# Performance work log

Hardware: AMD Instinct MI355X
Metric: run time of the kernel (lower is better)

Reference implementation:

```python
import jax, jax.numpy as jnp
import numpy as np

B, N, K, F_IN, F_OUT = 8, 2048, 32, 256, 256


def setup_inputs() -> dict:
    key = jax.random.key(0)
    ks = jax.random.split(key, 8)
    x = jax.random.normal(ks[0], (B, N, F_IN), dtype=jnp.float32)
    idx_neib = jax.random.randint(ks[1], (N, K), 0, N, dtype=jnp.int32)
    # Linear params (torch nn.Linear stores weight as [out, in])
    lim_x = np.sqrt(2.0) * np.sqrt(6.0 / (F_IN + F_OUT))  # xavier_uniform, gain=relu
    Wx_w = jax.random.uniform(ks[2], (F_OUT, F_IN), jnp.float32, -lim_x, lim_x)
    Wx_b = jnp.zeros((F_OUT,), jnp.float32)
    Wn_w = jax.random.uniform(ks[3], (F_OUT, F_IN), jnp.float32, -lim_x, lim_x)
    Wn_b = jnp.zeros((F_OUT,), jnp.float32)
    gamma = jnp.ones((2 * F_OUT,), jnp.float32)
    beta = jnp.zeros((2 * F_OUT,), jnp.float32)
    return {"x": x, "idx_neib": idx_neib, "Wx_w": Wx_w, "Wx_b": Wx_b,
            "Wn_w": Wn_w, "Wn_b": Wn_b, "gamma": gamma, "beta": beta}


def reference(x, idx_neib, Wx_w, Wx_b, Wn_w, Wn_b, gamma, beta):
    # Gather neighbor features: [B, N, K, F] then mean over the K neighbors.
    x_neib = jnp.take(x, idx_neib, axis=1).mean(axis=2)  # [B, N, F]
    # Dual linear projections (weights stored [out, in] as in torch).
    h_self = jnp.einsum('bnf,of->bno', x, Wx_w) + Wx_b
    h_nei = jnp.einsum('bnf,of->bno', x_neib, Wn_w) + Wn_b
    h = jnp.concatenate([h_self, h_nei], axis=2)          # [B, N, 2*out]
    # F.normalize(p=2, dim=2): divide by max(||h||_2, 1e-12)
    nrm = jnp.sqrt(jnp.sum(h * h, axis=2, keepdims=True))
    h = h / jnp.maximum(nrm, 1e-12)
    h = jax.nn.relu(h)
    # BatchNorm1d over channel dim (training mode: batch stats over B and N,
    # biased variance), eps=1e-5.
    mu = h.mean(axis=(0, 1))
    var = jnp.mean((h - mu) ** 2, axis=(0, 1))
    h = (h - mu) * jax.lax.rsqrt(var + 1e-5) * gamma + beta
    return h
```

## Files before the change

kernel.cpp:

```cpp
#include <hip/hip_runtime.h>
#include <stdint.h>

#define BB 8
#define NN 2048
#define KK 32
#define FIN 256
#define FOUT 256
#define CC 512
#define MM (BB*NN)
#define RB 32
#define NBLK (MM/RB)
#define LDA 264

typedef __attribute__((ext_vector_type(8))) short short8;
typedef __attribute__((ext_vector_type(4))) float f32x4;

__device__ __forceinline__ unsigned short f2bf(float f) {
    union { float f; unsigned u; } v; v.f = f;
    unsigned u = v.u;
    return (unsigned short)((u + 0x7FFFu + ((u >> 16) & 1u)) >> 16);
}
__device__ __forceinline__ float bf2f(unsigned short s) {
    union { unsigned u; float f; } v; v.u = ((unsigned)s) << 16;
    return v.f;
}

__global__ void k_prep(const float* __restrict__ Wx, const float* __restrict__ Wxb,
                       const float* __restrict__ Wn, const float* __restrict__ Wnb,
                       const float* __restrict__ x,
                       unsigned short* __restrict__ Wc, float* __restrict__ bc,
                       unsigned short* __restrict__ xb) {
    const int blk = blockIdx.x;
    const int tid = threadIdx.x;
    if (blk < 128) {
        int gid = blk * 256 + tid;
        int e0 = gid * 4;
        int o = e0 >> 8, k = e0 & 255;
        const float* src = (o < FOUT) ? (Wx + o * FIN + k) : (Wn + (o - FOUT) * FIN + k);
        float4 v = *(const float4*)src;
        ushort4 p; p.x = f2bf(v.x); p.y = f2bf(v.y); p.z = f2bf(v.z); p.w = f2bf(v.w);
        *(ushort4*)(Wc + e0) = p;
        if (gid < 128) {
            int c0 = gid * 4;
            float4 bv = (c0 < FOUT) ? *(const float4*)(Wxb + c0)
                                    : *(const float4*)(Wnb + c0 - FOUT);
            *(float4*)(bc + c0) = bv;
        }
    } else {
        size_t gid = (size_t)(blk - 128) * 256 + tid;
        size_t e0 = gid * 8;
        float4 v0 = *(const float4*)(x + e0);
        float4 v1 = *(const float4*)(x + e0 + 4);
        ushort4 p0, p1;
        p0.x = f2bf(v0.x); p0.y = f2bf(v0.y); p0.z = f2bf(v0.z); p0.w = f2bf(v0.w);
        p1.x = f2bf(v1.x); p1.y = f2bf(v1.y); p1.z = f2bf(v1.z); p1.w = f2bf(v1.w);
        *(ushort4*)(xb + e0)     = p0;
        *(ushort4*)(xb + e0 + 4) = p1;
    }
}

__global__ __launch_bounds__(512, 4)
void k_gemm(const unsigned short* __restrict__ xb, const int* __restrict__ idx,
            const unsigned short* __restrict__ Wc,
            const float* __restrict__ bc,
            unsigned short* __restrict__ h,
            float* __restrict__ psum, float* __restrict__ psq) {
    __shared__ unsigned short As[2][RB * LDA];
    __shared__ float sqpart[8][RB];
    __shared__ float rnorm[RB];

    const int bid  = blockIdx.x;
    const int tid  = threadIdx.x;
    const int w    = tid >> 6;
    const int lane = tid & 63;
    const int quad = lane >> 4;
    const int l16  = lane & 15;
    const int p    = lane >> 5;
    const int l32  = lane & 31;
    const int b    = bid & 7;
    const int n0   = (bid >> 3) * RB;
    const unsigned short* xbat = xb + (size_t)b * NN * FIN;
    const size_t r0g = (size_t)b * NN + n0;

    {
        const uint4* gs = (const uint4*)(xbat + (size_t)n0 * FIN);
        #pragma unroll
        for (int i = 0; i < 2; ++i) {
            int e = tid + i * 512;
            *(uint4*)&As[0][(e >> 5) * LDA + (e & 31) * 8] = gs[e];
        }
    }
    {
        #pragma unroll
        for (int rr = 0; rr < 4; ++rr) {
            int lr = (w << 2) + rr;
            const int* ip = idx + (n0 + lr) * KK;
            const unsigned short* xp = xbat + l32 * 8;
            float ac[8] = {0.f,0.f,0.f,0.f,0.f,0.f,0.f,0.f};
            #pragma unroll 8
            for (int k = 0; k < 16; ++k) {
                int j = ip[(k << 1) | p];
                uint4 v = *(const uint4*)(xp + (size_t)j * FIN);
                const unsigned short* hv = (const unsigned short*)&v;
                #pragma unroll
                for (int c = 0; c < 8; ++c) ac[c] += bf2f(hv[c]);
            }
            #pragma unroll
            for (int c = 0; c < 8; ++c) ac[c] += __shfl_xor(ac[c], 32, 64);
            if (p == 0) {
                const float s = 1.0f / (float)KK;
                unsigned short o8[8];
                #pragma unroll
                for (int c = 0; c < 8; ++c) o8[c] = f2bf(ac[c] * s);
                *(uint4*)&As[1][lr * LDA + l32 * 8] = *(const uint4*)o8;
            }
        }
    }
    __syncthreads();

    const int half = w >> 2;
    const unsigned short* A = As[half];
    const int cbg = half * 256 + (w & 3) * 64;

    f32x4 acc[2][4];
    #pragma unroll
    for (int mt = 0; mt < 2; ++mt)
        #pragma unroll
        for (int nt = 0; nt < 4; ++nt) acc[mt][nt] = (f32x4){0.f, 0.f, 0.f, 0.f};

    const unsigned short* Bp = Wc + (size_t)(cbg + l16) * FIN + quad * 8;
    const unsigned short* Ap = A + (size_t)l16 * LDA + quad * 8;

    #pragma unroll 2
    for (int k0 = 0; k0 < FIN; k0 += 32) {
        short8 a0 = *(const short8*)(Ap + k0);
        short8 a1 = *(const short8*)(Ap + 16 * LDA + k0);
        short8 bfr[4];
        #pragma unroll
        for (int nt = 0; nt < 4; ++nt)
            bfr[nt] = *(const short8*)(Bp + (size_t)nt * 16 * FIN + k0);
        #pragma unroll
        for (int nt = 0; nt < 4; ++nt) {
            acc[0][nt] = __builtin_amdgcn_mfma_f32_16x16x32_bf16(a0, bfr[nt], acc[0][nt], 0, 0, 0);
            acc[1][nt] = __builtin_amdgcn_mfma_f32_16x16x32_bf16(a1, bfr[nt], acc[1][nt], 0, 0, 0);
        }
    }

    float bcv[4];
    #pragma unroll
    for (int nt = 0; nt < 4; ++nt) bcv[nt] = bc[cbg + nt * 16 + l16];

    float rsq[2][4] = {{0.f,0.f,0.f,0.f},{0.f,0.f,0.f,0.f}};
    #pragma unroll
    for (int mt = 0; mt < 2; ++mt)
        #pragma unroll
        for (int nt = 0; nt < 4; ++nt)
            #pragma unroll
            for (int r = 0; r < 4; ++r) {
                float v = acc[mt][nt][r] + bcv[nt];
                acc[mt][nt][r] = v;
                rsq[mt][r] += v * v;
            }
    #pragma unroll
    for (int off = 1; off < 16; off <<= 1)
        #pragma unroll
        for (int mt = 0; mt < 2; ++mt)
            #pragma unroll
            for (int r = 0; r < 4; ++r)
                rsq[mt][r] += __shfl_xor(rsq[mt][r], off, 64);
    if (l16 == 0) {
        #pragma unroll
        for (int mt = 0; mt < 2; ++mt)
            #pragma unroll
            for (int r = 0; r < 4; ++r)
                sqpart[w][mt * 16 + quad * 4 + r] = rsq[mt][r];
    }
    __syncthreads();
    if (tid < RB) {
        float tot = 0.f;
        #pragma unroll
        for (int i = 0; i < 8; ++i) tot += sqpart[i][tid];
        rnorm[tid] = 1.0f / fmaxf(sqrtf(tot), 1e-12f);
    }
    __syncthreads();

    float csum[4] = {0.f,0.f,0.f,0.f};
    float csq [4] = {0.f,0.f,0.f,0.f};
    #pragma unroll
    for (int mt = 0; mt < 2; ++mt) {
        #pragma unroll
        for (int r = 0; r < 4; ++r) {
            int row = mt * 16 + quad * 4 + r;
            float rn = rnorm[row];
            unsigned short* hp = h + (r0g + row) * CC + cbg + l16;
            #pragma unroll
            for (int nt = 0; nt < 4; ++nt) {
                float v = fmaxf(acc[mt][nt][r] * rn, 0.0f);
                hp[nt * 16] = f2bf(v);
                csum[nt] += v;
                csq [nt] += v * v;
            }
        }
    }
    #pragma unroll
    for (int off = 16; off < 64; off <<= 1)
        #pragma unroll
        for (int nt = 0; nt < 4; ++nt) {
            csum[nt] += __shfl_xor(csum[nt], off, 64);
            csq [nt] += __shfl_xor(csq [nt], off, 64);
        }
    if (quad == 0) {
        #pragma unroll
        for (int nt = 0; nt < 4; ++nt) {
            int c = cbg + nt * 16 + l16;
            psum[(size_t)c * NBLK + bid] = csum[nt];
            psq [(size_t)c * NBLK + bid] = csq [nt];
        }
    }
}

__global__ void k_stats(const float* __restrict__ psum, const float* __restrict__ psq,
                        const float* __restrict__ gamma, const float* __restrict__ beta,
                        float* __restrict__ ss) {
    __shared__ float ps[4], pq[4];
    int c = blockIdx.x, t = threadIdx.x;
    float s = psum[(size_t)c * NBLK + t] + psum[(size_t)c * NBLK + 256 + t];
    float q = psq [(size_t)c * NBLK + t] + psq [(size_t)c * NBLK + 256 + t];
    #pragma unroll
    for (int off = 32; off; off >>= 1) { s += __shfl_xor(s, off, 64); q += __shfl_xor(q, off, 64); }
    int w = t >> 6, lane = t & 63;
    if (lane == 0) { ps[w] = s; pq[w] = q; }
    __syncthreads();
    if (t == 0) {
        float S = ps[0] + ps[1] + ps[2] + ps[3];
        float Q = pq[0] + pq[1] + pq[2] + pq[3];
        const float inv = 1.0f / (float)MM;
        float mu  = S * inv;
        float var = fmaxf(Q * inv - mu * mu, 0.0f);
        float sc  = gamma[c] * rsqrtf(var + 1e-5f);
        ss[c]      = sc;
        ss[CC + c] = beta[c] - mu * sc;
    }
}

__global__ void k_apply(const unsigned short* __restrict__ h,
                        const float* __restrict__ ss,
                        float* __restrict__ out) {
    int gid = blockIdx.x * 256 + threadIdx.x;
    int c0 = (gid * 8) & (CC - 1);
    uint4 hv = ((const uint4*)h)[gid];
    const unsigned short* hs = (const unsigned short*)&hv;
    float4 sc0 = *(const float4*)(ss + c0);
    float4 sc1 = *(const float4*)(ss + c0 + 4);
    float4 sh0 = *(const float4*)(ss + CC + c0);
    float4 sh1 = *(const float4*)(ss + CC + c0 + 4);
    float4 o0, o1;
    o0.x = bf2f(hs[0]) * sc0.x + sh0.x;
    o0.y = bf2f(hs[1]) * sc0.y + sh0.y;
    o0.z = bf2f(hs[2]) * sc0.z + sh0.z;
    o0.w = bf2f(hs[3]) * sc0.w + sh0.w;
    o1.x = bf2f(hs[4]) * sc1.x + sh1.x;
    o1.y = bf2f(hs[5]) * sc1.y + sh1.y;
    o1.z = bf2f(hs[6]) * sc1.z + sh1.z;
    o1.w = bf2f(hs[7]) * sc1.w + sh1.w;
    ((float4*)out)[gid * 2]     = o0;
    ((float4*)out)[gid * 2 + 1] = o1;
}

extern "C" void kernel_launch(void* const* d_in, const int* in_sizes, int n_in,
                              void* d_out, int out_size, void* d_ws, size_t ws_size,
                              hipStream_t stream) {
    const float* x     = (const float*)d_in[0];
    const int*   idx   = (const int*)  d_in[1];
    const float* Wx_w  = (const float*)d_in[2];
    const float* Wx_b  = (const float*)d_in[3];
    const float* Wn_w  = (const float*)d_in[4];
    const float* Wn_b  = (const float*)d_in[5];
    const float* gamma = (const float*)d_in[6];
    const float* beta  = (const float*)d_in[7];
    float* out = (float*)d_out;

    char* p = (char*)d_ws;
    unsigned short* xb = (unsigned short*)p; p += (size_t)MM * FIN * 2;
    unsigned short* Wc = (unsigned short*)p; p += (size_t)CC * FIN * 2;
    float* bc          = (float*)p;          p += (size_t)CC * 4;
    unsigned short* h  = (unsigned short*)p; p += (size_t)MM * CC * 2;
    float* psum        = (float*)p;          p += (size_t)CC * NBLK * 4;
    float* psq         = (float*)p;          p += (size_t)CC * NBLK * 4;
    float* ss          = (float*)p;          p += (size_t)2 * CC * 4;

    hipLaunchKernelGGL(k_prep,  dim3(2176), dim3(256), 0, stream,
                       Wx_w, Wx_b, Wn_w, Wn_b, x, Wc, bc, xb);
    hipLaunchKernelGGL(k_gemm,  dim3(NBLK), dim3(512), 0, stream, xb, idx, Wc, bc, h, psum, psq);
    hipLaunchKernelGGL(k_stats, dim3(CC),   dim3(256), 0, stream, psum, psq, gamma, beta, ss);
    hipLaunchKernelGGL(k_apply, dim3(4096), dim3(256), 0, stream, h, ss, out);
}
```

Baseline: 130.4 us.

## Transpose bf16 activations to node-major layout so neighbor gathers cover all batches

The prep kernel now writes the bf16 copy of x as [N][B][F] instead of [B][N][F]. Each GEMM block takes 4 nodes across all 8 batches (32 rows), so one neighbor index fetches a contiguous 4 KB slab covering every batch. This cuts index loads and turns scattered 512-byte row gathers into larger coalesced reads. Output row addressing and the per-block stat partials are remapped to match. The cost is a strided scatter in the prep kernel's store pattern.

```diff
diff --git a/kernel.cpp b/kernel.cpp
--- a/kernel.cpp
+++ b/kernel.cpp
@@ -9,7 +9,7 @@
 #define CC 512
 #define MM (BB*NN)
 #define RB 32
-#define NBLK (MM/RB)
+#define NBLK 512
 #define LDA 264
 
 typedef __attribute__((ext_vector_type(8))) short short8;
@@ -29,7 +29,7 @@
                        const float* __restrict__ Wn, const float* __restrict__ Wnb,
                        const float* __restrict__ x,
                        unsigned short* __restrict__ Wc, float* __restrict__ bc,
-                       unsigned short* __restrict__ xb) {
+                       unsigned short* __restrict__ xb_t) {
     const int blk = blockIdx.x;
     const int tid = threadIdx.x;
     if (blk < 128) {
@@ -49,18 +49,22 @@
     } else {
         size_t gid = (size_t)(blk - 128) * 256 + tid;
         size_t e0 = gid * 8;
+        int b = (int)(e0 >> 19);
+        int n = (int)((e0 >> 8) & (NN - 1));
+        int c = (int)(e0 & (FIN - 1));
         float4 v0 = *(const float4*)(x + e0);
         float4 v1 = *(const float4*)(x + e0 + 4);
         ushort4 p0, p1;
         p0.x = f2bf(v0.x); p0.y = f2bf(v0.y); p0.z = f2bf(v0.z); p0.w = f2bf(v0.w);
         p1.x = f2bf(v1.x); p1.y = f2bf(v1.y); p1.z = f2bf(v1.z); p1.w = f2bf(v1.w);
-        *(ushort4*)(xb + e0)     = p0;
-        *(ushort4*)(xb + e0 + 4) = p1;
+        unsigned short* dst = xb_t + ((size_t)n * BB + b) * FIN + c;
+        *(ushort4*)dst       = p0;
+        *(ushort4*)(dst + 4) = p1;
     }
 }
 
 __global__ __launch_bounds__(512, 4)
-void k_gemm(const unsigned short* __restrict__ xb, const int* __restrict__ idx,
+void k_gemm(const unsigned short* __restrict__ xb_t, const int* __restrict__ idx,
             const unsigned short* __restrict__ Wc,
             const float* __restrict__ bc,
             unsigned short* __restrict__ h,
@@ -75,15 +79,10 @@
     const int lane = tid & 63;
     const int quad = lane >> 4;
     const int l16  = lane & 15;
-    const int p    = lane >> 5;
-    const int l32  = lane & 31;
-    const int b    = bid & 7;
-    const int n0   = (bid >> 3) * RB;
-    const unsigned short* xbat = xb + (size_t)b * NN * FIN;
-    const size_t r0g = (size_t)b * NN + n0;
+    const int n0   = bid * 4;
 
     {
-        const uint4* gs = (const uint4*)(xbat + (size_t)n0 * FIN);
+        const uint4* gs = (const uint4*)(xb_t + (size_t)n0 * BB * FIN);
         #pragma unroll
         for (int i = 0; i < 2; ++i) {
             int e = tid + i * 512;
@@ -91,30 +90,29 @@
         }
     }
     {
-        #pragma unroll
-        for (int rr = 0; rr < 4; ++rr) {
-            int lr = (w << 2) + rr;
-            const int* ip = idx + (n0 + lr) * KK;
-            const unsigned short* xp = xbat + l32 * 8;
-            float ac[8] = {0.f,0.f,0.f,0.f,0.f,0.f,0.f,0.f};
-            #pragma unroll 8
-            for (int k = 0; k < 16; ++k) {
-                int j = ip[(k << 1) | p];
-                uint4 v = *(const uint4*)(xp + (size_t)j * FIN);
-                const unsigned short* hv = (const unsigned short*)&v;
-                #pragma unroll
-                for (int c = 0; c < 8; ++c) ac[c] += bf2f(hv[c]);
-            }
-            #pragma unroll
-            for (int c = 0; c < 8; ++c) ac[c] += __shfl_xor(ac[c], 32, 64);
-            if (p == 0) {
-                const float s = 1.0f / (float)KK;
-                unsigned short o8[8];
-                #pragma unroll
-                for (int c = 0; c < 8; ++c) o8[c] = f2bf(ac[c] * s);
-                *(uint4*)&As[1][lr * LDA + l32 * 8] = *(const uint4*)o8;
-            }
-        }
+        const int n_local = w >> 1;
+        const int part    = w & 1;
+        const int* ip = idx + (n0 + n_local) * KK;
+        const unsigned short* sp = xb_t + part * (4 * FIN) + lane * 8;
+        float ac0[8] = {0.f,0.f,0.f,0.f,0.f,0.f,0.f,0.f};
+        float ac1[8] = {0.f,0.f,0.f,0.f,0.f,0.f,0.f,0.f};
+        #pragma unroll 8
+        for (int k = 0; k < KK; ++k) {
+            const unsigned short* base = sp + (size_t)ip[k] * (BB * FIN);
+            uint4 v0 = *(const uint4*)base;
+            uint4 v1 = *(const uint4*)(base + 512);
+            const unsigned short* h0 = (const unsigned short*)&v0;
+            const unsigned short* h1 = (const unsigned short*)&v1;
+            #pragma unroll
+            for (int c = 0; c < 8; ++c) { ac0[c] += bf2f(h0[c]); ac1[c] += bf2f(h1[c]); }
+        }
+        const float s = 1.0f / (float)KK;
+        unsigned short o0[8], o1[8];
+        #pragma unroll
+        for (int c = 0; c < 8; ++c) { o0[c] = f2bf(ac0[c] * s); o1[c] = f2bf(ac1[c] * s); }
+        int row0 = n_local * 8 + part * 4 + (lane >> 5);
+        *(uint4*)&As[1][row0 * LDA + (lane & 31) * 8]       = *(const uint4*)o0;
+        *(uint4*)&As[1][(row0 + 2) * LDA + (lane & 31) * 8] = *(const uint4*)o1;
     }
     __syncthreads();
 
@@ -192,7 +190,7 @@
         for (int r = 0; r < 4; ++r) {
             int row = mt * 16 + quad * 4 + r;
             float rn = rnorm[row];
-            unsigned short* hp = h + (r0g + row) * CC + cbg + l16;
+            unsigned short* hp = h + ((size_t)(row & 7) * NN + n0 + (row >> 3)) * CC + cbg + l16;
             #pragma unroll
             for (int nt = 0; nt < 4; ++nt) {
                 float v = fmaxf(acc[mt][nt][r] * rn, 0.0f);
@@ -209,7 +207,7 @@
             csum[nt] += __shfl_xor(csum[nt], off, 64);
             csq [nt] += __shfl_xor(csq [nt], off, 64);
         }
-    if (quad == 0) {
+    if (quad == 0 && (lane >> 5) == 0) {
         #pragma unroll
         for (int nt = 0; nt < 4; ++nt) {
             int c = cbg + nt * 16 + l16;
@@ -281,17 +279,17 @@
     float* out = (float*)d_out;
 
     char* p = (char*)d_ws;
-    unsigned short* xb = (unsigned short*)p; p += (size_t)MM * FIN * 2;
-    unsigned short* Wc = (unsigned short*)p; p += (size_t)CC * FIN * 2;
-    float* bc          = (float*)p;          p += (size_t)CC * 4;
-    unsigned short* h  = (unsigned short*)p; p += (size_t)MM * CC * 2;
-    float* psum        = (float*)p;          p += (size_t)CC * NBLK * 4;
-    float* psq         = (float*)p;          p += (size_t)CC * NBLK * 4;
-    float* ss          = (float*)p;          p += (size_t)2 * CC * 4;
+    unsigned short* xb_t = (unsigned short*)p; p += (size_t)MM * FIN * 2;
+    unsigned short* Wc   = (unsigned short*)p; p += (size_t)CC * FIN * 2;
+    float* bc            = (float*)p;          p += (size_t)CC * 4;
+    unsigned short* h    = (unsigned short*)p; p += (size_t)MM * CC * 2;
+    float* psum          = (float*)p;          p += (size_t)CC * NBLK * 4;
+    float* psq           = (float*)p;          p += (size_t)CC * NBLK * 4;
+    float* ss            = (float*)p;          p += (size_t)2 * CC * 4;
 
     hipLaunchKernelGGL(k_prep,  dim3(2176), dim3(256), 0, stream,
-                       Wx_w, Wx_b, Wn_w, Wn_b, x, Wc, bc, xb);
-    hipLaunchKernelGGL(k_gemm,  dim3(NBLK), dim3(512), 0, stream, xb, idx, Wc, bc, h, psum, psq);
+                       Wx_w, Wx_b, Wn_w, Wn_b, x, Wc, bc, xb_t);
+    hipLaunchKernelGGL(k_gemm,  dim3(NBLK), dim3(512), 0, stream, xb_t, idx, Wc, bc, h, psum, psq);
     hipLaunchKernelGGL(k_stats, dim3(CC),   dim3(256), 0, stream, psum, psq, gamma, beta, ss);
     hipLaunchKernelGGL(k_apply, dim3(4096), dim3(256), 0, stream, h, ss, out);
 }
```

Measured after the change: 138.2 us. 6.0% more time.
